# Kernel optimization log

Hardware: AMD Instinct MI355X
Metric: run time of the kernel (lower is better)

The kernel has to match this reference:

```python
import jax, jax.numpy as jnp
import numpy as np
import math

N_HEAD = 16
N_EMBD = 2048
HEAD_DIM = 128
N_LAYER = 24
EPS = 1e-5


def _get_alibi_slopes(n_heads):
    def pow2(n):
        start = 2 ** (-2 ** (-(math.log2(n) - 3)))
        return [start * start ** i for i in range(n)]
    if math.log2(n_heads).is_integer():
        return pow2(n_heads)
    c = 2 ** math.floor(math.log2(n_heads))
    s = pow2(c)
    extra = _get_alibi_slopes(2 * c)
    return s + extra[0::2][: n_heads - c]

ALIBI_SLOPES = jnp.asarray(np.array(_get_alibi_slopes(N_HEAD), dtype=np.float32))  # (H,)


def rmsnorm(x, w, eps=EPS):
    # fp32 RMSNorm over last dim with affine weight (use_fp32=True path)
    xf = x.astype(jnp.float32)
    out = xf * jax.lax.rsqrt(jnp.mean(xf * xf, axis=-1, keepdims=True) + eps)
    return (out * w.astype(jnp.float32)).astype(x.dtype)


def setup_inputs() -> dict:
    key = jax.random.key(0)
    ks = jax.random.split(key, 8)
    B, T, C, H, D = 2, 2048, N_EMBD, N_HEAD, HEAD_DIM
    sc = 1.0 / math.sqrt(C)
    proj_std = 0.5 / math.sqrt(C) / math.sqrt(N_LAYER)
    return {
        "x": jax.random.normal(ks[0], (B, T, C), jnp.float32),
        "Wq": jax.random.normal(ks[1], (C, H * D), jnp.float32) * sc,
        "Wk": jax.random.normal(ks[2], (C, H * D), jnp.float32) * sc,
        "Wv": jax.random.normal(ks[3], (C, H * D), jnp.float32) * sc,
        "Wproj": jax.random.normal(ks[4], (H * D, C), jnp.float32) * proj_std,
        "q_rms_w": jnp.ones((D,), jnp.float32),
        "k_rms_w": jnp.ones((D,), jnp.float32),
        "subln_w": jnp.ones((D,), jnp.float32),
    }


def reference(x, Wq, Wk, Wv, Wproj, q_rms_w, k_rms_w, subln_w):
    B, T, C = x.shape
    H, D = N_HEAD, HEAD_DIM
    q = (x @ Wq).reshape(B, T, H, D)
    k = (x @ Wk).reshape(B, T, H, D)
    v = (x @ Wv).reshape(B, T, H, D)
    # QK RMSNorm over head_dim
    q = rmsnorm(q, q_rms_w)
    k = rmsnorm(k, k_rms_w)
    # ALiBi bias: -slope * max(i-j, 0), plus causal mask
    idx = jnp.arange(T)
    dist = jnp.maximum(idx[:, None] - idx[None, :], 0).astype(jnp.float32)  # (T,T)
    bias = -dist[None, :, :] * ALIBI_SLOPES[:, None, None]  # (H,T,T)
    causal = idx[:, None] >= idx[None, :]  # (T,T)
    scale = 1.0 / math.sqrt(D)
    scores = jnp.einsum("bthd,bshd->bhts", q, k) * scale + bias[None]  # (B,H,T,T)
    scores = jnp.where(causal[None, None], scores, -jnp.inf)
    attn = jax.nn.softmax(scores, axis=-1)
    y = jnp.einsum("bhts,bshd->bhtd", attn, v)  # (B,H,T,D)
    y = rmsnorm(y, subln_w)  # post-attention groupnorm (subln)
    y = y.transpose(0, 2, 1, 3).reshape(B, T, H * D)
    return y @ Wproj
```

## Files before the change

kernel.cpp:

```cpp
#include <hip/hip_runtime.h>
#include <hip/hip_bf16.h>

#define Bc 2
#define Tc 2048
#define Cc 2048
#define Hc 16
#define Dc 128
#define BTc 4096
#define NQ 6144
#define EPSc 1e-5f
#define QSCALE 0.08838834764831845f

typedef __attribute__((ext_vector_type(8))) short bf16x8;
typedef __attribute__((ext_vector_type(4))) short bf16x4;
typedef __attribute__((ext_vector_type(4))) float f32x4;

__device__ __forceinline__ f32x4 mfma16(bf16x8 a, bf16x8 b, f32x4 c) {
  return __builtin_amdgcn_mfma_f32_16x16x32_bf16(a, b, c, 0, 0, 0);
}

__device__ __forceinline__ void gload16(const void* g, void* l) {
  __builtin_amdgcn_global_load_lds(
      (const __attribute__((address_space(1))) void*)g,
      (__attribute__((address_space(3))) void*)l, 16, 0, 0);
}

__global__ __launch_bounds__(256) void k_xconv(const float* __restrict__ x,
                                               __hip_bfloat16* __restrict__ xb) {
  size_t i = ((size_t)blockIdx.x * 256 + threadIdx.x) * 4;
  float4 v = *(const float4*)(x + i);
  union { __hip_bfloat16 h[4]; bf16x4 v4; } u;
  u.h[0] = __float2bfloat16(v.x); u.h[1] = __float2bfloat16(v.y);
  u.h[2] = __float2bfloat16(v.z); u.h[3] = __float2bfloat16(v.w);
  *(bf16x4*)(xb + i) = u.v4;
}

__global__ __launch_bounds__(256) void k_wconv(const float* __restrict__ Wq,
    const float* __restrict__ Wk, const float* __restrict__ Wv,
    const float* __restrict__ Wp, __hip_bfloat16* __restrict__ Wqkv_t,
    __hip_bfloat16* __restrict__ Wproj_t) {
  __shared__ float tile[64][65];
  int z = blockIdx.z;
  const float* src = (z == 0) ? Wq : (z == 1) ? Wk : (z == 2) ? Wv : Wp;
  __hip_bfloat16* dst = (z < 3) ? (Wqkv_t + (size_t)z * Cc * Cc) : Wproj_t;
  int k0 = blockIdx.x * 64, n0 = blockIdx.y * 64;
  int c = threadIdx.x & 63, rb = threadIdx.x >> 6;
  for (int i = 0; i < 16; i++) {
    int r = rb * 16 + i;
    tile[r][c] = src[(size_t)(k0 + r) * Cc + n0 + c];
  }
  __syncthreads();
  for (int i = 0; i < 16; i++) {
    int r = rb * 16 + i;
    dst[(size_t)(n0 + r) * Cc + k0 + c] = __float2bfloat16(tile[c][r]);
  }
}

__device__ __forceinline__ void mm48(f32x4 (&acc)[4][8], const bf16x8 (&A_)[4],
                                     const bf16x8 (&B_)[8]) {
  __builtin_amdgcn_s_setprio(1);
#pragma unroll
  for (int m = 0; m < 4; m++)
#pragma unroll
    for (int n = 0; n < 8; n++)
      acc[m][n] = mfma16(A_[m], B_[n], acc[m][n]);
  __builtin_amdgcn_s_setprio(0);
}

template <typename OutT>
__global__ __launch_bounds__(256, 2) void k_gemm4(const __hip_bfloat16* __restrict__ A,
    const __hip_bfloat16* __restrict__ Bt, OutT* __restrict__ Co,
    int M, int N) {
  constexpr int K = 2048;
  __shared__ __align__(16) char lds[73728];
  const int nbx = M >> 7;
  const int nwg = nbx * (N >> 8);
  const int wg = blockIdx.x;
  const int swz = (wg & 7) * (nwg >> 3) + (wg >> 3);
  const int bx = swz % nbx, by = swz / nbx;
  const int tid = threadIdx.x, lane = tid & 63, wid = tid >> 6;
  const int wr = wid >> 1, wc = wid & 1;
  const int lr = lane & 15, lg = lane >> 4;
  const int xs = lg ^ ((lr >> 1) & 3);
  const int aoffR = (wr * 64 + lr) * 64 + xs * 16;
  const int boffR = 8192 + (wc * 128 + lr) * 64 + xs * 16;
  const int srow = lane >> 2;
  const int scolE = (((lane & 3) ^ ((lane >> 3) & 3)) << 3);
  const __hip_bfloat16* Ag = A + (size_t)(bx * 128 + wid * 32 + srow) * K + scolE;
  const __hip_bfloat16* Bg = Bt + (size_t)(by * 256 + wid * 64 + srow) * K + scolE;
  const size_t rK16 = (size_t)16 * K;
  char* dA = lds + wid * 2048;
  char* dB = lds + 8192 + wid * 4096;

#define STG(BUF, TS) {                                                   \
    gload16(Ag + (TS) * 32,        dA + (BUF) * 24576);                  \
    gload16(Ag + rK16 + (TS) * 32, dA + (BUF) * 24576 + 1024);           \
    gload16(Bg + (TS) * 32,            dB + (BUF) * 24576);              \
    gload16(Bg + rK16 + (TS) * 32,     dB + (BUF) * 24576 + 1024);       \
    gload16(Bg + 2 * rK16 + (TS) * 32, dB + (BUF) * 24576 + 2048);       \
    gload16(Bg + 3 * rK16 + (TS) * 32, dB + (BUF) * 24576 + 3072);       \
  }
#define BARRIER asm volatile("s_barrier" ::: "memory")
#define VW6 asm volatile("s_waitcnt vmcnt(6)" ::: "memory")
#define VW0 asm volatile("s_waitcnt vmcnt(0)" ::: "memory")

  f32x4 acc[4][8];
#pragma unroll
  for (int m = 0; m < 4; m++)
#pragma unroll
    for (int n = 0; n < 8; n++) acc[m][n] = f32x4{0.f, 0.f, 0.f, 0.f};
  bf16x8 rA[4], rB[8];

#define PH(RB, SB, TS, DOSTG, ENDW) {                                    \
    _Pragma("unroll")                                                    \
    for (int m = 0; m < 4; m++)                                          \
      rA[m] = *(const bf16x8*)(lds + (RB) * 24576 + aoffR + m * 1024);   \
    _Pragma("unroll")                                                    \
    for (int n = 0; n < 8; n++)                                          \
      rB[n] = *(const bf16x8*)(lds + (RB) * 24576 + boffR + n * 1024);   \
    if (DOSTG) STG((SB), (TS));                                          \
    mm48(acc, rA, rB);                                                   \
    ENDW;                                                                \
    BARRIER;                                                             \
  }

  STG(0, 0); STG(1, 1);
  VW6;
  BARRIER;

  for (int i = 0; i < 20; ++i) {
    const int t = 3 * i;
    PH(0, 2, t + 2, 1, VW6);
    PH(1, 0, t + 3, 1, VW6);
    PH(2, 1, t + 4, 1, VW6);
  }
  PH(0, 2, 62, 1, VW6);
  PH(1, 0, 63, 1, VW6);
  PH(2, 0, 0, 0, VW0);
  PH(0, 0, 0, 0, (void)0);
#undef PH
#undef STG
#undef BARRIER
#undef VW6
#undef VW0

  const int row0 = bx * 128 + wr * 64 + lg * 4;
  const int col0 = by * 256 + wc * 128 + lr;
#pragma unroll
  for (int m = 0; m < 4; m++)
#pragma unroll
    for (int n = 0; n < 8; n++) {
      size_t base = (size_t)(row0 + m * 16) * N + col0 + n * 16;
#pragma unroll
      for (int r = 0; r < 4; r++) {
        float v = acc[m][n][r];
        if constexpr (sizeof(OutT) == 2)
          Co[base + (size_t)r * N] = __float2bfloat16(v);
        else
          Co[base + (size_t)r * N] = v;
      }
    }
}

__device__ __forceinline__ void rdA4(bf16x8 (&d)[4], const char* p) {
#pragma unroll
  for (int m = 0; m < 4; m++) d[m] = *(const bf16x8*)(p + m * 1024);
}
__device__ __forceinline__ void rdB4(bf16x8 (&d)[4], const char* p) {
#pragma unroll
  for (int n = 0; n < 4; n++) d[n] = *(const bf16x8*)(p + n * 1024);
}
__device__ __forceinline__ void mm44(f32x4 (&acc)[4][4], const bf16x8 (&A_)[4],
                                     const bf16x8 (&B_)[4]) {
  __builtin_amdgcn_s_setprio(1);
#pragma unroll
  for (int m = 0; m < 4; m++)
#pragma unroll
    for (int n = 0; n < 4; n++)
      acc[m][n] = mfma16(A_[m], B_[n], acc[m][n]);
  __builtin_amdgcn_s_setprio(0);
}

template <typename OutT>
__global__ __launch_bounds__(512, 2) void k_gemm8b(const __hip_bfloat16* __restrict__ A,
    const __hip_bfloat16* __restrict__ Bt, OutT* __restrict__ Co,
    int M, int N) {
  constexpr int K = 2048;
  __shared__ __align__(16) char lds[147456];
  const int nbx = M >> 7;
  const int nwg = nbx * (N >> 8);
  const int wg = blockIdx.x;
  const int swz = (wg & 7) * (nwg >> 3) + (wg >> 3);
  const int bx = swz % nbx, by = swz / nbx;
  const int tid = threadIdx.x, lane = tid & 63, wid = tid >> 6;
  const int wr = wid >> 2, wc = wid & 3;
  const int lr = lane & 15, lg = lane >> 4;
  const int roff = lr * 64 + (lg ^ ((lr >> 1) & 3)) * 16;
  const int srow = wid * 16 + (lane >> 2);
  const int scol = (((lane & 3) ^ ((srow >> 1) & 3)) << 3);
  const __hip_bfloat16* Ag = A + (size_t)(bx * 128 + srow) * K + scol;
  const __hip_bfloat16* Bg = Bt + (size_t)(by * 256 + srow) * K + scol;
  char* ldsw = lds + wid * 1024;
  const size_t rstepB = (size_t)128 * K;
  const char* Ab = lds + wr * 4096 + roff;
  const char* Bb = lds + 16384 + wc * 4096 + roff;

#define STG_A(bufo, t, kk) gload16(Ag + (t) * 64 + (kk) * 32, \
                                   ldsw + (bufo) + (kk) * 8192)
#define STG_B(bufo, t, kk) { const __hip_bfloat16* g_ = Bg + (t) * 64 + (kk) * 32; \
    gload16(g_, ldsw + (bufo) + 16384 + (kk) * 16384);                              \
    gload16(g_ + rstepB, ldsw + (bufo) + 16384 + (kk) * 16384 + 8192); }
#define BARRIER asm volatile("s_barrier" ::: "memory")
#define VW6 asm volatile("s_waitcnt vmcnt(6)" ::: "memory")
#define VW0 asm volatile("s_waitcnt vmcnt(0)" ::: "memory")

  f32x4 acc[4][4];
#pragma unroll
  for (int m = 0; m < 4; m++)
#pragma unroll
    for (int n = 0; n < 4; n++) acc[m][n] = f32x4{0.f, 0.f, 0.f, 0.f};
  bf16x8 rA[4], rB[4];

#define TILE(RB, SB, TS, DOSTG, ENDW)                                   \
  {                                                                     \
    rdA4(rA, Ab + (RB));                                                \
    rdB4(rB, Bb + (RB));                                                \
    if (DOSTG) { STG_A((SB), (TS), 0); STG_B((SB), (TS), 0); }          \
    BARRIER;                                                            \
    mm44(acc, rA, rB);                                                  \
    BARRIER;                                                            \
    rdA4(rA, Ab + (RB) + 8192);                                         \
    rdB4(rB, Bb + (RB) + 16384);                                        \
    if (DOSTG) { STG_A((SB), (TS), 1); STG_B((SB), (TS), 1); }          \
    BARRIER;                                                            \
    mm44(acc, rA, rB);                                                  \
    ENDW;                                                               \
    BARRIER;                                                            \
  }

  STG_A(0, 0, 0); STG_B(0, 0, 0); STG_A(0, 0, 1); STG_B(0, 0, 1);
  STG_A(49152, 1, 0); STG_B(49152, 1, 0); STG_A(49152, 1, 1); STG_B(49152, 1, 1);
  VW6;
  BARRIER;

  for (int i = 0; i < 10; ++i) {
    const int t = 3 * i;
    TILE(0,     98304, t + 2, 1, VW6);
    TILE(49152, 0,     t + 3, 1, VW6);
    TILE(98304, 49152, t + 4, 1, VW6);
  }
  TILE(0,     0, 0, 0, VW0);
  TILE(49152, 0, 0, 0, (void)0);
#undef TILE
#undef STG_A
#undef STG_B
#undef BARRIER
#undef VW6
#undef VW0

  const int row0 = bx * 128 + wr * 64 + lg * 4;
  const int col0 = by * 256 + wc * 64 + lr;
#pragma unroll
  for (int m = 0; m < 4; m++)
#pragma unroll
    for (int n = 0; n < 4; n++) {
      size_t base = (size_t)(row0 + m * 16) * N + col0 + n * 16;
#pragma unroll
      for (int r = 0; r < 4; r++) {
        float v = acc[m][n][r];
        if constexpr (sizeof(OutT) == 2)
          Co[base + (size_t)r * N] = __float2bfloat16(v);
        else
          Co[base + (size_t)r * N] = v;
      }
    }
}

__global__ __launch_bounds__(256) void k_qkrms(__hip_bfloat16* __restrict__ QKV,
    const float* __restrict__ qw, const float* __restrict__ kw) {
  int bt = blockIdx.x;
  int w = threadIdx.x >> 6, lane = threadIdx.x & 63;
  int hv = blockIdx.y * 4 + w;
  const float* wt; int col; float extra;
  if (hv < 16) { wt = qw; col = hv * Dc;             extra = QSCALE; }
  else         { wt = kw; col = Cc + (hv - 16) * Dc; extra = 1.0f;   }
  __hip_bfloat16* p = QKV + (size_t)bt * NQ + col + lane * 2;
  float x0 = __bfloat162float(p[0]);
  float x1 = __bfloat162float(p[1]);
  float ss = x0 * x0 + x1 * x1;
  for (int m = 1; m < 64; m <<= 1) ss += __shfl_xor(ss, m);
  float sc = rsqrtf(ss * (1.0f / Dc) + EPSc) * extra;
  p[0] = __float2bfloat16(x0 * sc * wt[lane * 2]);
  p[1] = __float2bfloat16(x1 * sc * wt[lane * 2 + 1]);
}

__global__ __launch_bounds__(256) void k_vtrans(const __hip_bfloat16* __restrict__ QKV,
                                                __hip_bfloat16* __restrict__ Vt) {
  __shared__ __hip_bfloat16 tile[64][65];
  int bh = blockIdx.z, t0 = blockIdx.x * 64, d0 = blockIdx.y * 64;
  int b = bh >> 4, h = bh & 15;
  int c = threadIdx.x & 63, rb = threadIdx.x >> 6;
  for (int i = 0; i < 16; i++) {
    int r = rb * 16 + i;
    tile[r][c] = QKV[(size_t)(b * Tc + t0 + r) * NQ + 2 * Cc + h * Dc + d0 + c];
  }
  __syncthreads();
  for (int i = 0; i < 16; i++) {
    int r = rb * 16 + i;
    Vt[((size_t)bh * Dc + d0 + r) * Tc + t0 + c] = tile[c][r];
  }
}

__global__ __launch_bounds__(256, 2) void k_attn(const __hip_bfloat16* __restrict__ QKV,
    const __hip_bfloat16* __restrict__ Vt, const float* __restrict__ subw,
    __hip_bfloat16* __restrict__ Y) {
  __shared__ __align__(16) __hip_bfloat16 Ks[2][64][128];
  __shared__ __align__(16) __hip_bfloat16 Vs[2][128][64];
  __shared__ __align__(16) __hip_bfloat16 Plds[4][16][72];
  const int bh = blockIdx.x, pp = blockIdx.y;
  const int b = bh >> 4, h = bh & 15;
  const int w = threadIdx.x >> 6, lane = threadIdx.x & 63;
  const int lr = lane & 15, lg = lane >> 4;
  const float slope = exp2f(-0.5f * (float)(h + 1));
  const __hip_bfloat16* Kbase = QKV + (size_t)b * Tc * NQ + Cc + h * Dc;
  const __hip_bfloat16* Vbase = Vt + (size_t)bh * Dc * Tc;
  const int krow = (lane >> 4);
  const int kcolb = ((lane & 15) << 4);
  const int vrow = (lane >> 3);
  const int vcolb = ((lane & 7) << 4);
  f32x4 zero = {0.f, 0.f, 0.f, 0.f};

#define STAGE(bb, t)                                                              \
    {                                                                             \
      const int s0_ = (t) * 64;                                                   \
      for (int j = 0; j < 4; j++) {                                               \
        int row = w * 16 + j * 4 + krow;                                          \
        int cb = kcolb ^ ((row & 7) << 4);                                        \
        gload16(Kbase + (size_t)(s0_ + row) * NQ + (cb >> 1),                     \
                &Ks[bb][w * 16 + j * 4][0]);                                      \
      }                                                                           \
      for (int j = 0; j < 4; j++) {                                               \
        int row = w * 32 + j * 8 + vrow;                                          \
        int cb = vcolb ^ ((row & 7) << 4);                                        \
        gload16(Vbase + (size_t)row * Tc + s0_ + (cb >> 1),                       \
                &Vs[bb][w * 32 + j * 8][0]);                                      \
      }                                                                           \
    }
#define SBAR asm volatile("s_barrier" ::: "memory")
#define AVW8 asm volatile("s_waitcnt vmcnt(8)" ::: "memory")
#define AVW0 asm volatile("s_waitcnt vmcnt(0)" ::: "memory")
#define ALG0 asm volatile("s_waitcnt lgkmcnt(0)" ::: "memory")

  int buf = 0;
  for (int ti = 0; ti < 2; ti++) {
    const int qt = (ti == 0) ? (31 - pp) : pp;
    const int q0 = qt * 64 + w * 16;
    const int nchunk = qt + 1;
    bf16x8 aq[4];
    {
      const __hip_bfloat16* qb = QKV + (size_t)(b * Tc + q0 + lr) * NQ + h * Dc + lg * 8;
      for (int c = 0; c < 4; c++) aq[c] = *(const bf16x8*)(qb + c * 32);
    }
    f32x4 acc[8];
    for (int d = 0; d < 8; d++) acc[d] = zero;
    float mrow[4] = {-1e30f, -1e30f, -1e30f, -1e30f};
    float lrow[4] = {0.f, 0.f, 0.f, 0.f};

    SBAR;
    STAGE(buf, 0);
    for (int t = 0; t < nchunk; t++) {
      if (t + 1 < nchunk) { STAGE(buf ^ 1, t + 1); AVW8; }
      else                { AVW0; }
      SBAR;
      const int s0 = t * 64;
      f32x4 s[4];
      for (int ss = 0; ss < 4; ss++) s[ss] = zero;
      __builtin_amdgcn_s_setprio(1);
      for (int c = 0; c < 4; c++)
        for (int ss = 0; ss < 4; ss++) {
          int kr = ss * 16 + lr;
          const bf16x8 kf = *(const bf16x8*)
              &Ks[buf][kr][((c * 64 + lg * 16) ^ ((kr & 7) << 4)) >> 1];
          s[ss] = mfma16(aq[c], kf, s[ss]);
        }
      __builtin_amdgcn_s_setprio(0);
      float ps[4][4], mt[4];
      for (int r = 0; r < 4; r++) mt[r] = -1e30f;
      for (int ss = 0; ss < 4; ss++) {
        int jj = s0 + ss * 16 + lr;
        for (int r = 0; r < 4; r++) {
          int i = q0 + lg * 4 + r;
          float pv = (jj <= i) ? s[ss][r] - slope * (float)(i - jj) : -1e30f;
          ps[ss][r] = pv;
          mt[r] = fmaxf(mt[r], pv);
        }
      }
      for (int m = 1; m < 16; m <<= 1)
        for (int r = 0; r < 4; r++) mt[r] = fmaxf(mt[r], __shfl_xor(mt[r], m));
      float corr[4], rs[4];
      for (int r = 0; r < 4; r++) {
        float mn = fmaxf(mrow[r], mt[r]);
        corr[r] = __expf(mrow[r] - mn);
        mrow[r] = mn;
        rs[r] = 0.f;
      }
      for (int ss = 0; ss < 4; ss++)
        for (int r = 0; r < 4; r++) {
          float e = __expf(ps[ss][r] - mrow[r]);
          ps[ss][r] = e;
          rs[r] += e;
        }
      for (int m = 1; m < 16; m <<= 1)
        for (int r = 0; r < 4; r++) rs[r] += __shfl_xor(rs[r], m);
      for (int r = 0; r < 4; r++) lrow[r] = lrow[r] * corr[r] + rs[r];
      for (int d = 0; d < 8; d++)
        for (int r = 0; r < 4; r++) acc[d][r] *= corr[r];
      for (int ss = 0; ss < 4; ss++)
        for (int r = 0; r < 4; r++)
          Plds[w][lg * 4 + r][ss * 16 + lr] = __float2bfloat16(ps[ss][r]);
      bf16x8 pa0 = *(const bf16x8*)&Plds[w][lr][lg * 8];
      bf16x8 pa1 = *(const bf16x8*)&Plds[w][lr][32 + lg * 8];
      __builtin_amdgcn_s_setprio(1);
      for (int d = 0; d < 8; d++) {
        int vr = d * 16 + lr;
        const bf16x8 b0 = *(const bf16x8*)
            &Vs[buf][vr][((lg * 16) ^ ((vr & 7) << 4)) >> 1];
        const bf16x8 b1 = *(const bf16x8*)
            &Vs[buf][vr][((64 + lg * 16) ^ ((vr & 7) << 4)) >> 1];
        acc[d] = mfma16(pa0, b0, acc[d]);
        acc[d] = mfma16(pa1, b1, acc[d]);
      }
      __builtin_amdgcn_s_setprio(0);
      ALG0; SBAR;
      buf ^= 1;
    }
    float ssum[4] = {0.f, 0.f, 0.f, 0.f};
    for (int r = 0; r < 4; r++) {
      float rl = 1.0f / lrow[r];
      for (int d = 0; d < 8; d++) {
        float o = acc[d][r] * rl;
        acc[d][r] = o;
        ssum[r] += o * o;
      }
    }
    for (int m = 1; m < 16; m <<= 1)
      for (int r = 0; r < 4; r++) ssum[r] += __shfl_xor(ssum[r], m);
    float ms[4];
    for (int r = 0; r < 4; r++) ms[r] = rsqrtf(ssum[r] * (1.0f / Dc) + EPSc);
    for (int d = 0; d < 8; d++) {
      float wv = subw[d * 16 + lr];
      for (int r = 0; r < 4; r++) {
        float y = acc[d][r] * ms[r] * wv;
        Y[(size_t)(b * Tc + q0 + lg * 4 + r) * Cc + h * Dc + d * 16 + lr] =
            __float2bfloat16(y);
      }
    }
  }
#undef STAGE
#undef SBAR
#undef AVW8
#undef AVW0
#undef ALG0
}

extern "C" void kernel_launch(void* const* d_in, const int* in_sizes, int n_in,
                              void* d_out, int out_size, void* d_ws, size_t ws_size,
                              hipStream_t stream) {
  const float* x  = (const float*)d_in[0];
  const float* Wq = (const float*)d_in[1];
  const float* Wk = (const float*)d_in[2];
  const float* Wv = (const float*)d_in[3];
  const float* Wp = (const float*)d_in[4];
  const float* qw = (const float*)d_in[5];
  const float* kw = (const float*)d_in[6];
  const float* sw = (const float*)d_in[7];
  float* out = (float*)d_out;

  char* ws = (char*)d_ws;
  __hip_bfloat16* Xb    = (__hip_bfloat16*)(ws + 0);
  __hip_bfloat16* Wqkv  = (__hip_bfloat16*)(ws + 16777216);
  __hip_bfloat16* Wproj = (__hip_bfloat16*)(ws + 41943040);
  __hip_bfloat16* QKV   = (__hip_bfloat16*)(ws + 50331648);
  __hip_bfloat16* Vt    = (__hip_bfloat16*)(ws + 100663296);
  __hip_bfloat16* Yb    = (__hip_bfloat16*)(ws + 117440512);

  k_xconv<<<dim3((BTc * Cc) / 1024), 256, 0, stream>>>(x, Xb);
  k_wconv<<<dim3(32, 32, 4), 256, 0, stream>>>(Wq, Wk, Wv, Wp, Wqkv, Wproj);
  k_gemm4<__hip_bfloat16><<<dim3((BTc / 128) * (NQ / 256)), 256, 0, stream>>>(
      Xb, Wqkv, QKV, BTc, NQ);
  k_qkrms<<<dim3(BTc, 8), 256, 0, stream>>>(QKV, qw, kw);
  k_vtrans<<<dim3(Tc / 64, Dc / 64, Bc * Hc), 256, 0, stream>>>(QKV, Vt);
  k_attn<<<dim3(Bc * Hc, 16), 256, 0, stream>>>(QKV, Vt, sw, Yb);
  k_gemm8b<float><<<dim3((BTc / 128) * (Cc / 256)), 512, 0, stream>>>(
      Yb, Wproj, out, BTc, Cc);
}
```

Before: 279.8 us.

## Fuse QK RMSNorm and V transpose into QKV GEMM epilogue; reuse gemm4 for proj

Moves the per-head RMSNorm for Q and K into the QKV GEMM epilogue, using cross-lane shuffles over each 128-column head tile. V is written straight out in transposed layout. This removes the separate k_qkrms and k_vtrans kernels and their extra global read/write passes over QKV. The output projection now uses the 256-thread k_gemm4 instead of the 512-thread k_gemm8b. The transposed V stores are 8-byte scattered writes, and the projection GEMM's efficiency may differ with the different kernel.

```diff
diff --git a/kernel.cpp b/kernel.cpp
--- a/kernel.cpp
+++ b/kernel.cpp
@@ -14,6 +14,8 @@
 typedef __attribute__((ext_vector_type(8))) short bf16x8;
 typedef __attribute__((ext_vector_type(4))) short bf16x4;
 typedef __attribute__((ext_vector_type(4))) float f32x4;
+
+typedef struct { unsigned short u[4]; } us4;
 
 __device__ __forceinline__ f32x4 mfma16(bf16x8 a, bf16x8 b, f32x4 c) {
   return __builtin_amdgcn_mfma_f32_16x16x32_bf16(a, b, c, 0, 0, 0);
@@ -67,10 +69,11 @@
   __builtin_amdgcn_s_setprio(0);
 }
 
-template <typename OutT>
+template <int MODE, typename OutT>
 __global__ __launch_bounds__(256, 2) void k_gemm4(const __hip_bfloat16* __restrict__ A,
     const __hip_bfloat16* __restrict__ Bt, OutT* __restrict__ Co,
-    int M, int N) {
+    int M, int N, const float* __restrict__ qw, const float* __restrict__ kw,
+    __hip_bfloat16* __restrict__ Vt) {
   constexpr int K = 2048;
   __shared__ __align__(16) char lds[73728];
   const int nbx = M >> 7;
@@ -146,168 +149,74 @@
 
   const int row0 = bx * 128 + wr * 64 + lg * 4;
   const int col0 = by * 256 + wc * 128 + lr;
-#pragma unroll
-  for (int m = 0; m < 4; m++)
-#pragma unroll
-    for (int n = 0; n < 8; n++) {
-      size_t base = (size_t)(row0 + m * 16) * N + col0 + n * 16;
-#pragma unroll
-      for (int r = 0; r < 4; r++) {
-        float v = acc[m][n][r];
-        if constexpr (sizeof(OutT) == 2)
-          Co[base + (size_t)r * N] = __float2bfloat16(v);
-        else
-          Co[base + (size_t)r * N] = v;
-      }
-    }
-}
-
-__device__ __forceinline__ void rdA4(bf16x8 (&d)[4], const char* p) {
-#pragma unroll
-  for (int m = 0; m < 4; m++) d[m] = *(const bf16x8*)(p + m * 1024);
-}
-__device__ __forceinline__ void rdB4(bf16x8 (&d)[4], const char* p) {
-#pragma unroll
-  for (int n = 0; n < 4; n++) d[n] = *(const bf16x8*)(p + n * 1024);
-}
-__device__ __forceinline__ void mm44(f32x4 (&acc)[4][4], const bf16x8 (&A_)[4],
-                                     const bf16x8 (&B_)[4]) {
-  __builtin_amdgcn_s_setprio(1);
-#pragma unroll
-  for (int m = 0; m < 4; m++)
-#pragma unroll
-    for (int n = 0; n < 4; n++)
-      acc[m][n] = mfma16(A_[m], B_[n], acc[m][n]);
-  __builtin_amdgcn_s_setprio(0);
-}
-
-template <typename OutT>
-__global__ __launch_bounds__(512, 2) void k_gemm8b(const __hip_bfloat16* __restrict__ A,
-    const __hip_bfloat16* __restrict__ Bt, OutT* __restrict__ Co,
-    int M, int N) {
-  constexpr int K = 2048;
-  __shared__ __align__(16) char lds[147456];
-  const int nbx = M >> 7;
-  const int nwg = nbx * (N >> 8);
-  const int wg = blockIdx.x;
-  const int swz = (wg & 7) * (nwg >> 3) + (wg >> 3);
-  const int bx = swz % nbx, by = swz / nbx;
-  const int tid = threadIdx.x, lane = tid & 63, wid = tid >> 6;
-  const int wr = wid >> 2, wc = wid & 3;
-  const int lr = lane & 15, lg = lane >> 4;
-  const int roff = lr * 64 + (lg ^ ((lr >> 1) & 3)) * 16;
-  const int srow = wid * 16 + (lane >> 2);
-  const int scol = (((lane & 3) ^ ((srow >> 1) & 3)) << 3);
-  const __hip_bfloat16* Ag = A + (size_t)(bx * 128 + srow) * K + scol;
-  const __hip_bfloat16* Bg = Bt + (size_t)(by * 256 + srow) * K + scol;
-  char* ldsw = lds + wid * 1024;
-  const size_t rstepB = (size_t)128 * K;
-  const char* Ab = lds + wr * 4096 + roff;
-  const char* Bb = lds + 16384 + wc * 4096 + roff;
-
-#define STG_A(bufo, t, kk) gload16(Ag + (t) * 64 + (kk) * 32, \
-                                   ldsw + (bufo) + (kk) * 8192)
-#define STG_B(bufo, t, kk) { const __hip_bfloat16* g_ = Bg + (t) * 64 + (kk) * 32; \
-    gload16(g_, ldsw + (bufo) + 16384 + (kk) * 16384);                              \
-    gload16(g_ + rstepB, ldsw + (bufo) + 16384 + (kk) * 16384 + 8192); }
-#define BARRIER asm volatile("s_barrier" ::: "memory")
-#define VW6 asm volatile("s_waitcnt vmcnt(6)" ::: "memory")
-#define VW0 asm volatile("s_waitcnt vmcnt(0)" ::: "memory")
-
-  f32x4 acc[4][4];
-#pragma unroll
-  for (int m = 0; m < 4; m++)
-#pragma unroll
-    for (int n = 0; n < 4; n++) acc[m][n] = f32x4{0.f, 0.f, 0.f, 0.f};
-  bf16x8 rA[4], rB[4];
-
-#define TILE(RB, SB, TS, DOSTG, ENDW)                                   \
-  {                                                                     \
-    rdA4(rA, Ab + (RB));                                                \
-    rdB4(rB, Bb + (RB));                                                \
-    if (DOSTG) { STG_A((SB), (TS), 0); STG_B((SB), (TS), 0); }          \
-    BARRIER;                                                            \
-    mm44(acc, rA, rB);                                                  \
-    BARRIER;                                                            \
-    rdA4(rA, Ab + (RB) + 8192);                                         \
-    rdB4(rB, Bb + (RB) + 16384);                                        \
-    if (DOSTG) { STG_A((SB), (TS), 1); STG_B((SB), (TS), 1); }          \
-    BARRIER;                                                            \
-    mm44(acc, rA, rB);                                                  \
-    ENDW;                                                               \
-    BARRIER;                                                            \
-  }
-
-  STG_A(0, 0, 0); STG_B(0, 0, 0); STG_A(0, 0, 1); STG_B(0, 0, 1);
-  STG_A(49152, 1, 0); STG_B(49152, 1, 0); STG_A(49152, 1, 1); STG_B(49152, 1, 1);
-  VW6;
-  BARRIER;
-
-  for (int i = 0; i < 10; ++i) {
-    const int t = 3 * i;
-    TILE(0,     98304, t + 2, 1, VW6);
-    TILE(49152, 0,     t + 3, 1, VW6);
-    TILE(98304, 49152, t + 4, 1, VW6);
-  }
-  TILE(0,     0, 0, 0, VW0);
-  TILE(49152, 0, 0, 0, (void)0);
-#undef TILE
-#undef STG_A
-#undef STG_B
-#undef BARRIER
-#undef VW6
-#undef VW0
-
-  const int row0 = bx * 128 + wr * 64 + lg * 4;
-  const int col0 = by * 256 + wc * 64 + lr;
-#pragma unroll
-  for (int m = 0; m < 4; m++)
-#pragma unroll
-    for (int n = 0; n < 4; n++) {
-      size_t base = (size_t)(row0 + m * 16) * N + col0 + n * 16;
-#pragma unroll
-      for (int r = 0; r < 4; r++) {
-        float v = acc[m][n][r];
-        if constexpr (sizeof(OutT) == 2)
-          Co[base + (size_t)r * N] = __float2bfloat16(v);
-        else
-          Co[base + (size_t)r * N] = v;
-      }
-    }
-}
-
-__global__ __launch_bounds__(256) void k_qkrms(__hip_bfloat16* __restrict__ QKV,
-    const float* __restrict__ qw, const float* __restrict__ kw) {
-  int bt = blockIdx.x;
-  int w = threadIdx.x >> 6, lane = threadIdx.x & 63;
-  int hv = blockIdx.y * 4 + w;
-  const float* wt; int col; float extra;
-  if (hv < 16) { wt = qw; col = hv * Dc;             extra = QSCALE; }
-  else         { wt = kw; col = Cc + (hv - 16) * Dc; extra = 1.0f;   }
-  __hip_bfloat16* p = QKV + (size_t)bt * NQ + col + lane * 2;
-  float x0 = __bfloat162float(p[0]);
-  float x1 = __bfloat162float(p[1]);
-  float ss = x0 * x0 + x1 * x1;
-  for (int m = 1; m < 64; m <<= 1) ss += __shfl_xor(ss, m);
-  float sc = rsqrtf(ss * (1.0f / Dc) + EPSc) * extra;
-  p[0] = __float2bfloat16(x0 * sc * wt[lane * 2]);
-  p[1] = __float2bfloat16(x1 * sc * wt[lane * 2 + 1]);
-}
-
-__global__ __launch_bounds__(256) void k_vtrans(const __hip_bfloat16* __restrict__ QKV,
-                                                __hip_bfloat16* __restrict__ Vt) {
-  __shared__ __hip_bfloat16 tile[64][65];
-  int bh = blockIdx.z, t0 = blockIdx.x * 64, d0 = blockIdx.y * 64;
-  int b = bh >> 4, h = bh & 15;
-  int c = threadIdx.x & 63, rb = threadIdx.x >> 6;
-  for (int i = 0; i < 16; i++) {
-    int r = rb * 16 + i;
-    tile[r][c] = QKV[(size_t)(b * Tc + t0 + r) * NQ + 2 * Cc + h * Dc + d0 + c];
-  }
-  __syncthreads();
-  for (int i = 0; i < 16; i++) {
-    int r = rb * 16 + i;
-    Vt[((size_t)bh * Dc + d0 + r) * Tc + t0 + c] = tile[c][r];
+
+  if (MODE == 1) {
+    const int region = by >> 3;
+    if (region < 2) {
+      const float* wsel = (region == 0) ? qw : kw;
+      const float extra = (region == 0) ? QSCALE : 1.0f;
+      float wv[8];
+#pragma unroll
+      for (int n = 0; n < 8; n++) wv[n] = wsel[n * 16 + lr];
+#pragma unroll
+      for (int m = 0; m < 4; m++) {
+        float ss[4] = {0.f, 0.f, 0.f, 0.f};
+#pragma unroll
+        for (int n = 0; n < 8; n++)
+#pragma unroll
+          for (int r = 0; r < 4; r++) ss[r] += acc[m][n][r] * acc[m][n][r];
+        for (int msk = 1; msk < 16; msk <<= 1)
+#pragma unroll
+          for (int r = 0; r < 4; r++) ss[r] += __shfl_xor(ss[r], msk);
+        float sc[4];
+#pragma unroll
+        for (int r = 0; r < 4; r++)
+          sc[r] = rsqrtf(ss[r] * (1.0f / Dc) + EPSc) * extra;
+#pragma unroll
+        for (int n = 0; n < 8; n++) {
+          size_t base = (size_t)(row0 + m * 16) * N + col0 + n * 16;
+#pragma unroll
+          for (int r = 0; r < 4; r++)
+            ((__hip_bfloat16*)Co)[base + (size_t)r * N] =
+                __float2bfloat16(acc[m][n][r] * sc[r] * wv[n]);
+        }
+      }
+    } else {
+      const int h = ((by - 16) * 256 + wc * 128) >> 7;
+      const int bat = bx >> 4;
+#pragma unroll
+      for (int m = 0; m < 4; m++) {
+        const int t0 = (row0 + m * 16) & (Tc - 1);
+#pragma unroll
+        for (int n = 0; n < 8; n++) {
+          union { us4 p; unsigned long long q; } u;
+#pragma unroll
+          for (int r = 0; r < 4; r++) {
+            union { __hip_bfloat16 h16; unsigned short s; } cv;
+            cv.h16 = __float2bfloat16(acc[m][n][r]);
+            u.p.u[r] = cv.s;
+          }
+          __hip_bfloat16* dst = Vt +
+              ((size_t)(bat * 16 + h) * 128 + n * 16 + lr) * Tc + t0;
+          *(unsigned long long*)dst = u.q;
+        }
+      }
+    }
+  } else {
+#pragma unroll
+    for (int m = 0; m < 4; m++)
+#pragma unroll
+      for (int n = 0; n < 8; n++) {
+        size_t base = (size_t)(row0 + m * 16) * N + col0 + n * 16;
+#pragma unroll
+        for (int r = 0; r < 4; r++) {
+          float v = acc[m][n][r];
+          if constexpr (sizeof(OutT) == 2)
+            Co[base + (size_t)r * N] = __float2bfloat16(v);
+          else
+            Co[base + (size_t)r * N] = v;
+        }
+      }
   }
 }
 
@@ -486,11 +395,9 @@
 
   k_xconv<<<dim3((BTc * Cc) / 1024), 256, 0, stream>>>(x, Xb);
   k_wconv<<<dim3(32, 32, 4), 256, 0, stream>>>(Wq, Wk, Wv, Wp, Wqkv, Wproj);
-  k_gemm4<__hip_bfloat16><<<dim3((BTc / 128) * (NQ / 256)), 256, 0, stream>>>(
-      Xb, Wqkv, QKV, BTc, NQ);
-  k_qkrms<<<dim3(BTc, 8), 256, 0, stream>>>(QKV, qw, kw);
-  k_vtrans<<<dim3(Tc / 64, Dc / 64, Bc * Hc), 256, 0, stream>>>(QKV, Vt);
+  k_gemm4<1, __hip_bfloat16><<<dim3((BTc / 128) * (NQ / 256)), 256, 0, stream>>>(
+      Xb, Wqkv, QKV, BTc, NQ, qw, kw, Vt);
   k_attn<<<dim3(Bc * Hc, 16), 256, 0, stream>>>(QKV, Vt, sw, Yb);
-  k_gemm8b<float><<<dim3((BTc / 128) * (Cc / 256)), 512, 0, stream>>>(
-      Yb, Wproj, out, BTc, Cc);
-}
+  k_gemm4<0, float><<<dim3((BTc / 128) * (Cc / 256)), 256, 0, stream>>>(
+      Yb, Wproj, out, BTc, Cc, nullptr, nullptr, nullptr);
+}
```

Measured after the change: 262.0 us. -6.4%, faster.
